# Optimization experiments

Measured on AMD Instinct MI355X. Metric: run time of the kernel, lower is better.

## Reference

```python
import jax, jax.numpy as jnp
import numpy as np

N, E = 50000, 800000
IN, EIN, HID, OUT = 128, 64, 64, 64
NEG_SLOPE = 0.2


def setup_inputs() -> dict:
    key = jax.random.key(0)
    ks = jax.random.split(key, 24)
    p = lambda k, shape: jax.random.normal(k, shape, jnp.float32) * 0.05
    return {
        'x': jax.random.normal(ks[0], (N, IN), jnp.float32),
        'edge_index': jax.random.randint(ks[1], (2, E), 0, N, jnp.int64),
        'edge_attr': jax.random.normal(ks[2], (E, EIN), jnp.float32),
        'batch': jnp.sort(jax.random.randint(ks[3], (N,), 0, 64, jnp.int64)),
        # GATConv 1 (in -> hidden, edge_dim=EIN)
        'W1': p(ks[4], (IN, HID)), 'a_src1': p(ks[5], (HID,)), 'a_dst1': p(ks[6], (HID,)),
        'We1': p(ks[7], (EIN, HID)), 'a_e1': p(ks[8], (HID,)), 'b1': jnp.zeros((HID,), jnp.float32),
        # GATConv 2 (hidden -> out)
        'W2': p(ks[9], (HID, OUT)), 'a_src2': p(ks[10], (OUT,)), 'a_dst2': p(ks[11], (OUT,)),
        'We2': p(ks[12], (EIN, OUT)), 'a_e2': p(ks[13], (OUT,)), 'b2': jnp.zeros((OUT,), jnp.float32),
        # edge MLP
        'Wm1': p(ks[14], (EIN, HID)), 'bm1': jnp.zeros((HID,), jnp.float32),
        'Wm2': p(ks[15], (HID, OUT)), 'bm2': jnp.zeros((OUT,), jnp.float32),
    }


def _gat(x, src, dst, edge_attr, W, a_s, a_d, We, a_e, b, n):
    # PyG GATConv (heads=1): add self-loops with edge_attr fill_value='mean'
    ones = jnp.ones((src.shape[0],), x.dtype)
    deg = jax.ops.segment_sum(ones, dst, num_segments=n)
    loop_attr = jax.ops.segment_sum(edge_attr, dst, num_segments=n) / jnp.maximum(deg, 1.0)[:, None]
    ar = jnp.arange(n)
    src2 = jnp.concatenate([src, ar])
    dst2 = jnp.concatenate([dst, ar])
    ea = jnp.concatenate([edge_attr, loop_attr], axis=0)  # [E+N, EIN]
    h = x @ W                                             # [N, C]
    a_src = h @ a_s                                       # [N]
    a_dst = h @ a_d                                       # [N]
    a_edge = (ea @ We) @ a_e                              # [E+N]
    alpha = jax.nn.leaky_relu(a_src[src2] + a_dst[dst2] + a_edge, NEG_SLOPE)
    # scatter-softmax over incoming edges of each dst node
    amax = jax.ops.segment_max(alpha, dst2, num_segments=n)
    ex = jnp.exp(alpha - amax[dst2])
    denom = jax.ops.segment_sum(ex, dst2, num_segments=n)
    coef = ex / denom[dst2]                               # [E+N]
    out = jax.ops.segment_sum(h[src2] * coef[:, None], dst2, num_segments=n)
    return out + b


def reference(x, edge_index, edge_attr, batch,
              W1, a_src1, a_dst1, We1, a_e1, b1,
              W2, a_src2, a_dst2, We2, a_e2, b2,
              Wm1, bm1, Wm2, bm2):
    n = x.shape[0]
    src, dst = edge_index[0], edge_index[1]
    h = _gat(x, src, dst, edge_attr, W1, a_src1, a_dst1, We1, a_e1, b1, n)
    h = jax.nn.elu(h)
    h = _gat(h, src, dst, edge_attr, W2, a_src2, a_dst2, We2, a_e2, b2, n)
    e = jax.nn.relu(edge_attr @ Wm1 + bm1) @ Wm2 + bm2
    return h, e, batch
```

## Files before the change

### kernel.cpp

```cpp
#include <hip/hip_runtime.h>

constexpr int NN = 50000;
constexpr int NE = 800000;
constexpr int C = 64;
constexpr int IN_DIM = 128;
constexpr float NEG = 0.2f;
constexpr int NB = (NN + 255) / 256;

typedef __attribute__((ext_vector_type(8))) short short8;
typedef __attribute__((ext_vector_type(4))) float f32x4;

__device__ __forceinline__ unsigned short f2bf(float f) {
    unsigned u = __float_as_uint(f);
    unsigned r = 0x7FFFu + ((u >> 16) & 1u);
    return (unsigned short)((u + r) >> 16);
}
__device__ __forceinline__ unsigned pack_bf2(float a, float b) {
    return (unsigned)f2bf(a) | ((unsigned)f2bf(b) << 16);
}
__device__ __forceinline__ float bf2f(unsigned u) {
    return __uint_as_float(u << 16);
}

__global__ void k_zero(int* __restrict__ p, int n) {
    int t = blockIdx.x * blockDim.x + threadIdx.x;
    if (t < n) p[t] = 0;
}

__global__ void k_vecs(const float* __restrict__ We1, const float* __restrict__ ae1v,
                       const float* __restrict__ We2, const float* __restrict__ ae2v,
                       const float* __restrict__ W1, const float* __restrict__ as1,
                       const float* __restrict__ ad1,
                       const float* __restrict__ W2, const float* __restrict__ as2,
                       const float* __restrict__ ad2,
                       float* __restrict__ out) {
    int t = blockIdx.x * blockDim.x + threadIdx.x;
    const float* M; const float* v; int row;
    if      (t < 64)  { M = We1; v = ae1v; row = t; }
    else if (t < 128) { M = We2; v = ae2v; row = t - 64; }
    else if (t < 256) { M = W1;  v = as1;  row = t - 128; }
    else if (t < 384) { M = W1;  v = ad1;  row = t - 256; }
    else if (t < 448) { M = W2;  v = as2;  row = t - 384; }
    else              { M = W2;  v = ad2;  row = t - 448; }
    float s = 0.f;
    #pragma unroll
    for (int c = 0; c < 64; ++c) s += M[row * 64 + c] * v[c];
    out[t] = s;
}

__global__ __launch_bounds__(256) void k_mlp_mfma(
        const float* __restrict__ ea, const int* __restrict__ dst,
        const float* __restrict__ Wm1, const float* __restrict__ bm1,
        const float* __restrict__ Wm2, const float* __restrict__ bm2,
        const float* __restrict__ wv,
        float* __restrict__ eout, float* __restrict__ ae1, float* __restrict__ ae2,
        int* __restrict__ hist) {
    constexpr int AP = 144;
    __shared__ char Atile[128 * AP];
    __shared__ char Bt1[64 * AP];
    __shared__ char Bt2[64 * AP];
    const int t = threadIdx.x;
    const long long E0 = (long long)blockIdx.x * 128;
    const int l = t & 63;

    if (t < 128) atomicAdd(&hist[dst[E0 + t]], 1);

    {
        const int j = t & 15;
        const int eb = t >> 4;
        float4 wk1 = *(const float4*)&wv[j * 4];
        float4 wk2 = *(const float4*)&wv[64 + j * 4];
        const f32x4* g = (const f32x4*)(ea + E0 * 64);
        float s1[8], s2[8];
        #pragma unroll
        for (int q = 0; q < 8; ++q) {
            f32x4 v = __builtin_nontemporal_load(&g[t + 256 * q]);
            int e = eb + 16 * q;
            s1[q] = v[0] * wk1.x + v[1] * wk1.y + v[2] * wk1.z + v[3] * wk1.w;
            s2[q] = v[0] * wk2.x + v[1] * wk2.y + v[2] * wk2.z + v[3] * wk2.w;
            uint2 wr;
            wr.x = pack_bf2(v[0], v[1]);
            wr.y = pack_bf2(v[2], v[3]);
            *(uint2*)(Atile + e * AP + j * 8) = wr;
        }
        #pragma unroll
        for (int off = 1; off < 16; off <<= 1) {
            #pragma unroll
            for (int q = 0; q < 8; ++q) {
                s1[q] += __shfl_xor(s1[q], off);
                s2[q] += __shfl_xor(s2[q], off);
            }
        }
        float o1 = 0.f, o2 = 0.f;
        #pragma unroll
        for (int q = 0; q < 8; ++q) {
            if (j == q)     o1 = s1[q];
            if (j == q + 8) o2 = s2[q];
        }
        if (j < 8) ae1[E0 + eb + 16 * j] = o1;
        else       ae2[E0 + eb + 16 * (j - 8)] = o2;
    }
    {
        const int c = t & 63, kq = t >> 6;
        #pragma unroll
        for (int i = 0; i < 16; i += 2) {
            int k = kq * 16 + i;
            *(unsigned*)(Bt1 + c * AP + k * 2) = pack_bf2(Wm1[k * 64 + c], Wm1[(k + 1) * 64 + c]);
            *(unsigned*)(Bt2 + c * AP + k * 2) = pack_bf2(Wm2[k * 64 + c], Wm2[(k + 1) * 64 + c]);
        }
    }
    __syncthreads();

    const int m0 = (t >> 6) * 32;
    const int lr = l & 15;
    const int lq = l >> 4;
    const int lk = lq * 8;

    f32x4 acc[4][2] = {};
    #pragma unroll
    for (int ks = 0; ks < 2; ++ks) {
        int ko = ks * 32 + lk;
        short8 a0 = *(const short8*)(Atile + (m0 + lr) * AP + ko * 2);
        short8 a1 = *(const short8*)(Atile + (m0 + 16 + lr) * AP + ko * 2);
        #pragma unroll
        for (int ct = 0; ct < 4; ++ct) {
            short8 b = *(const short8*)(Bt1 + (ct * 16 + lr) * AP + ko * 2);
            acc[ct][0] = __builtin_amdgcn_mfma_f32_16x16x32_bf16(b, a0, acc[ct][0], 0, 0, 0);
            acc[ct][1] = __builtin_amdgcn_mfma_f32_16x16x32_bf16(b, a1, acc[ct][1], 0, 0, 0);
        }
    }
    #pragma unroll
    for (int ct = 0; ct < 4; ++ct) {
        float4 bv = *(const float4*)&bm1[ct * 16 + lq * 4];
        #pragma unroll
        for (int et = 0; et < 2; ++et) {
            float v0 = fmaxf(acc[ct][et][0] + bv.x, 0.f);
            float v1 = fmaxf(acc[ct][et][1] + bv.y, 0.f);
            float v2 = fmaxf(acc[ct][et][2] + bv.z, 0.f);
            float v3 = fmaxf(acc[ct][et][3] + bv.w, 0.f);
            uint2 w;
            w.x = pack_bf2(v0, v1);
            w.y = pack_bf2(v2, v3);
            int e = m0 + et * 16 + lr;
            *(uint2*)(Atile + e * AP + (ct * 16 + lq * 4) * 2) = w;
        }
    }
    f32x4 acc2[4][2] = {};
    #pragma unroll
    for (int ks = 0; ks < 2; ++ks) {
        int ko = ks * 32 + lk;
        short8 a0 = *(const short8*)(Atile + (m0 + lr) * AP + ko * 2);
        short8 a1 = *(const short8*)(Atile + (m0 + 16 + lr) * AP + ko * 2);
        #pragma unroll
        for (int ct = 0; ct < 4; ++ct) {
            short8 b = *(const short8*)(Bt2 + (ct * 16 + lr) * AP + ko * 2);
            acc2[ct][0] = __builtin_amdgcn_mfma_f32_16x16x32_bf16(b, a0, acc2[ct][0], 0, 0, 0);
            acc2[ct][1] = __builtin_amdgcn_mfma_f32_16x16x32_bf16(b, a1, acc2[ct][1], 0, 0, 0);
        }
    }
    #pragma unroll
    for (int ct = 0; ct < 4; ++ct) {
        float4 bv = *(const float4*)&bm2[ct * 16 + lq * 4];
        #pragma unroll
        for (int et = 0; et < 2; ++et) {
            int e = m0 + et * 16 + lr;
            f32x4 o;
            o[0] = acc2[ct][et][0] + bv.x;
            o[1] = acc2[ct][et][1] + bv.y;
            o[2] = acc2[ct][et][2] + bv.z;
            o[3] = acc2[ct][et][3] + bv.w;
            __builtin_nontemporal_store(o, (f32x4*)&eout[(E0 + e) * 64 + ct * 16 + lq * 4]);
        }
    }
}

template <int K>
__global__ __launch_bounds__(256) void k_feat_mfma(
        const float* __restrict__ x, const float* __restrict__ W,
        const float* __restrict__ uv,
        unsigned short* __restrict__ h, float* __restrict__ asrc,
        float* __restrict__ adst, int M) {
    constexpr int AP = K * 2 + 16;
    constexpr int QW = K / 4;
    constexpr int NQ = K / 8;
    constexpr int EPQ = 256 / QW;
    __shared__ char Atile[128 * AP];
    __shared__ char Bt[64 * AP];
    const int t = threadIdx.x;
    const int M0 = blockIdx.x * 128;
    const int l = t & 63;

    {
        const int j = t % QW;
        const int eb = t / QW;
        float4 wk1 = *(const float4*)&uv[j * 4];
        float4 wk2 = *(const float4*)&uv[K + j * 4];
        const float4* g = (const float4*)(x + (long long)M0 * K);
        float s1[NQ], s2[NQ];
        #pragma unroll
        for (int q = 0; q < NQ; ++q) {
            int e = eb + EPQ * q;
            float4 v = make_float4(0.f, 0.f, 0.f, 0.f);
            if (M0 + e < M) v = g[t + 256 * q];
            s1[q] = v.x * wk1.x + v.y * wk1.y + v.z * wk1.z + v.w * wk1.w;
            s2[q] = v.x * wk2.x + v.y * wk2.y + v.z * wk2.z + v.w * wk2.w;
            uint2 wr;
            wr.x = pack_bf2(v.x, v.y);
            wr.y = pack_bf2(v.z, v.w);
            *(uint2*)(Atile + e * AP + j * 8) = wr;
        }
        #pragma unroll
        for (int off = 1; off < QW; off <<= 1) {
            #pragma unroll
            for (int q = 0; q < NQ; ++q) {
                s1[q] += __shfl_xor(s1[q], off);
                s2[q] += __shfl_xor(s2[q], off);
            }
        }
        float o1 = 0.f, o2 = 0.f;
        #pragma unroll
        for (int q = 0; q < NQ; ++q) {
            if (j == q)      o1 = s1[q];
            if (j == q + NQ) o2 = s2[q];
        }
        if (j < NQ) { int e = eb + EPQ * j;        if (M0 + e < M) asrc[M0 + e] = o1; }
        else        { int e = eb + EPQ * (j - NQ); if (M0 + e < M) adst[M0 + e] = o2; }
    }
    {
        const int c = t & 63, kq = t >> 6;
        #pragma unroll
        for (int i = 0; i < K / 4; i += 2) {
            int k = kq * (K / 4) + i;
            *(unsigned*)(Bt + c * AP + k * 2) = pack_bf2(W[k * 64 + c], W[(k + 1) * 64 + c]);
        }
    }
    __syncthreads();

    const int m0 = (t >> 6) * 32;
    const int lr = l & 15;
    const int lq = l >> 4;
    const int lk = lq * 8;

    f32x4 acc[4][2] = {};
    #pragma unroll
    for (int ks = 0; ks < K / 32; ++ks) {
        int ko = ks * 32 + lk;
        short8 a0 = *(const short8*)(Atile + (m0 + lr) * AP + ko * 2);
        short8 a1 = *(const short8*)(Atile + (m0 + 16 + lr) * AP + ko * 2);
        #pragma unroll
        for (int ct = 0; ct < 4; ++ct) {
            short8 b = *(const short8*)(Bt + (ct * 16 + lr) * AP + ko * 2);
            acc[ct][0] = __builtin_amdgcn_mfma_f32_16x16x32_bf16(b, a0, acc[ct][0], 0, 0, 0);
            acc[ct][1] = __builtin_amdgcn_mfma_f32_16x16x32_bf16(b, a1, acc[ct][1], 0, 0, 0);
        }
    }
    #pragma unroll
    for (int ct = 0; ct < 4; ++ct)
    #pragma unroll
    for (int et = 0; et < 2; ++et) {
        int row = m0 + et * 16 + lr;
        if (M0 + row < M) {
            uint2 w;
            w.x = pack_bf2(acc[ct][et][0], acc[ct][et][1]);
            w.y = pack_bf2(acc[ct][et][2], acc[ct][et][3]);
            *(uint2*)&h[(long long)(M0 + row) * 64 + ct * 16 + lq * 4] = w;
        }
    }
}

__global__ void k_scan1(const int* __restrict__ hist, int* __restrict__ row_ptr,
                        int* __restrict__ bsum) {
    __shared__ int s[256];
    int t = threadIdx.x;
    int idx = blockIdx.x * 256 + t;
    int v = (idx < NN) ? hist[idx] : 0;
    s[t] = v;
    __syncthreads();
    #pragma unroll
    for (int off = 1; off < 256; off <<= 1) {
        int x = (t >= off) ? s[t - off] : 0;
        __syncthreads();
        s[t] += x;
        __syncthreads();
    }
    if (idx < NN) row_ptr[idx] = s[t] - v;
    if (t == 255) bsum[blockIdx.x] = s[255];
}

__global__ void k_scan2(int* __restrict__ bsum) {
    __shared__ int s[256];
    int t = threadIdx.x;
    int v = (t < NB) ? bsum[t] : 0;
    s[t] = v;
    __syncthreads();
    #pragma unroll
    for (int off = 1; off < 256; off <<= 1) {
        int x = (t >= off) ? s[t - off] : 0;
        __syncthreads();
        s[t] += x;
        __syncthreads();
    }
    if (t < NB) bsum[t] = s[t] - v;
}

__global__ void k_scan3(const int* __restrict__ bsum, int* __restrict__ row_ptr,
                        int* __restrict__ cursor) {
    int idx = blockIdx.x * 256 + threadIdx.x;
    if (idx < NN) {
        int r = row_ptr[idx] + bsum[blockIdx.x];
        row_ptr[idx] = r;
        cursor[idx] = r;
    }
    if (idx == 0) row_ptr[NN] = NE;
}

__global__ void k_scatter(const int* __restrict__ src, const int* __restrict__ dst,
                          const float* __restrict__ ae1, const float* __restrict__ ae2,
                          int* __restrict__ cursor, uint2* __restrict__ csr) {
    int t = blockIdx.x * blockDim.x + threadIdx.x;
    if (t >= NE) return;
    int d = dst[t];
    int pos = atomicAdd(&cursor[d], 1);
    csr[pos] = make_uint2((unsigned)src[t], pack_bf2(ae1[t], ae2[t]));
}

template <bool IS_L1>
__global__ void k_gat(const int* __restrict__ row_ptr, const uint2* __restrict__ csr,
                      const float* __restrict__ asrc, const float* __restrict__ adst,
                      const unsigned short* __restrict__ h, const float* __restrict__ bias,
                      float* __restrict__ out) {
    int n = blockIdx.x * 4 + (threadIdx.x >> 6);
    if (n >= NN) return;
    int lane = threadIdx.x & 63;
    int g = lane >> 4, s = lane & 15;
    int beg = row_ptr[n], end = row_ptr[n + 1];
    float adn = adst[n];
    float m = -1e30f, l = 0.f, sum_ae = 0.f;
    float4 acc = make_float4(0.f, 0.f, 0.f, 0.f);

    int i = beg + g;
    uint2 rc = make_uint2(0u, 0u);
    ushort4 hu = make_ushort4(0, 0, 0, 0);
    float asv = 0.f;
    if (i < end) {
        rc = csr[i];
        hu = *(const ushort4*)&h[(long long)rc.x * 64 + s * 4];
        asv = asrc[rc.x];
    }
    for (; i < end; i += 4) {
        uint2 rn = rc; ushort4 hn = hu; float asn = asv;
        if (i + 4 < end) {
            rn = csr[i + 4];
            hn = *(const ushort4*)&h[(long long)rn.x * 64 + s * 4];
            asn = asrc[rn.x];
        }
        float ae = IS_L1 ? bf2f(rc.y & 0xFFFFu) : bf2f(rc.y >> 16);
        sum_ae += ae;
        float a = asv + adn + ae;
        a = a > 0.f ? a : NEG * a;
        float mn = fmaxf(m, a);
        float sc = __expf(m - mn), p = __expf(a - mn);
        l = l * sc + p;
        acc.x = acc.x * sc + p * bf2f(hu.x);
        acc.y = acc.y * sc + p * bf2f(hu.y);
        acc.z = acc.z * sc + p * bf2f(hu.z);
        acc.w = acc.w * sc + p * bf2f(hu.w);
        m = mn;
        rc = rn; hu = hn; asv = asn;
    }
    #pragma unroll
    for (int off = 16; off < 64; off <<= 1) {
        float mo = __shfl_xor(m, off);
        float lo = __shfl_xor(l, off);
        float ax = __shfl_xor(acc.x, off);
        float ay = __shfl_xor(acc.y, off);
        float az = __shfl_xor(acc.z, off);
        float aw = __shfl_xor(acc.w, off);
        float so = __shfl_xor(sum_ae, off);
        float mn = fmaxf(m, mo);
        float s1 = __expf(m - mn), s2 = __expf(mo - mn);
        l = l * s1 + lo * s2;
        acc.x = acc.x * s1 + ax * s2;
        acc.y = acc.y * s1 + ay * s2;
        acc.z = acc.z * s1 + az * s2;
        acc.w = acc.w * s1 + aw * s2;
        sum_ae += so;
        m = mn;
    }
    {
        float deg = (float)(end - beg);
        float ae = sum_ae / fmaxf(deg, 1.f);
        float a = asrc[n] + adn + ae;
        a = a > 0.f ? a : NEG * a;
        ushort4 hun = *(const ushort4*)&h[(long long)n * 64 + s * 4];
        float mn = fmaxf(m, a);
        float sc = __expf(m - mn), p = __expf(a - mn);
        l = l * sc + p;
        acc.x = acc.x * sc + p * bf2f(hun.x);
        acc.y = acc.y * sc + p * bf2f(hun.y);
        acc.z = acc.z * sc + p * bf2f(hun.z);
        acc.w = acc.w * sc + p * bf2f(hun.w);
    }
    if (g == 0) {
        float4 o;
        o.x = acc.x / l + bias[s * 4 + 0];
        o.y = acc.y / l + bias[s * 4 + 1];
        o.z = acc.z / l + bias[s * 4 + 2];
        o.w = acc.w / l + bias[s * 4 + 3];
        if (IS_L1) {
            o.x = o.x > 0.f ? o.x : expm1f(o.x);
            o.y = o.y > 0.f ? o.y : expm1f(o.y);
            o.z = o.z > 0.f ? o.z : expm1f(o.z);
            o.w = o.w > 0.f ? o.w : expm1f(o.w);
        }
        *(float4*)&out[(long long)n * 64 + s * 4] = o;
    }
}

__global__ void k_batch(const int* __restrict__ batch, float* __restrict__ out) {
    int t = blockIdx.x * blockDim.x + threadIdx.x;
    if (t >= NN) return;
    out[t] = (float)batch[t];
}

extern "C" void kernel_launch(void* const* d_in, const int* in_sizes, int n_in,
                              void* d_out, int out_size, void* d_ws, size_t ws_size,
                              hipStream_t stream) {
    const float* x     = (const float*)d_in[0];
    const int*   eidx  = (const int*)d_in[1];
    const float* eattr = (const float*)d_in[2];
    const int*   batch = (const int*)d_in[3];
    const float* W1 = (const float*)d_in[4];
    const float* as1 = (const float*)d_in[5];
    const float* ad1 = (const float*)d_in[6];
    const float* We1 = (const float*)d_in[7];
    const float* vae1 = (const float*)d_in[8];
    const float* b1  = (const float*)d_in[9];
    const float* W2 = (const float*)d_in[10];
    const float* as2 = (const float*)d_in[11];
    const float* ad2 = (const float*)d_in[12];
    const float* We2 = (const float*)d_in[13];
    const float* vae2 = (const float*)d_in[14];
    const float* b2  = (const float*)d_in[15];
    const float* Wm1 = (const float*)d_in[16];
    const float* bm1 = (const float*)d_in[17];
    const float* Wm2 = (const float*)d_in[18];
    const float* bm2 = (const float*)d_in[19];

    const int* src = eidx;
    const int* dst = eidx + NE;

    float* out_h = (float*)d_out;
    float* out_e = out_h + (long long)NN * C;
    float* out_b = out_e + (long long)NE * C;

    uint2* csr    = (uint2*)d_ws;
    float* ae1    = (float*)(csr + NE);
    float* ae2    = ae1 + NE;
    float* out1   = ae2 + NE;
    unsigned short* h = (unsigned short*)(out1 + (long long)NN * C);
    float* asrc   = (float*)(h + (long long)NN * C);
    float* adst   = asrc + NN;
    float* vecs   = adst + NN;
    int*   hist   = (int*)(vecs + 512);
    int*   row_ptr= hist + NN;
    int*   cursor = row_ptr + NN + 1;
    int*   bsum   = cursor + NN;

    k_zero<<<NB, 256, 0, stream>>>(hist, NN);

    k_vecs<<<2, 256, 0, stream>>>(We1, vae1, We2, vae2, W1, as1, ad1, W2, as2, ad2, vecs);

    k_mlp_mfma<<<NE / 128, 256, 0, stream>>>(eattr, dst, Wm1, bm1, Wm2, bm2, vecs,
                                             out_e, ae1, ae2, hist);

    k_scan1<<<NB, 256, 0, stream>>>(hist, row_ptr, bsum);
    k_scan2<<<1, 256, 0, stream>>>(bsum);
    k_scan3<<<NB, 256, 0, stream>>>(bsum, row_ptr, cursor);
    k_scatter<<<(NE + 255) / 256, 256, 0, stream>>>(src, dst, ae1, ae2, cursor, csr);

    k_feat_mfma<IN_DIM><<<(NN + 127) / 128, 256, 0, stream>>>(x, W1, vecs + 128,
                                                              h, asrc, adst, NN);
    k_gat<true><<<(NN + 3) / 4, 256, 0, stream>>>(row_ptr, csr, asrc, adst, h, b1, out1);

    k_feat_mfma<C><<<(NN + 127) / 128, 256, 0, stream>>>(out1, W2, vecs + 384,
                                                         h, asrc, adst, NN);
    k_gat<false><<<(NN + 3) / 4, 256, 0, stream>>>(row_ptr, csr, asrc, adst, h, b2, out_h);

    k_batch<<<(NN + 255) / 256, 256, 0, stream>>>(batch, out_b);
}
```

Before: 279.8 us.

## Fuse setup kernels, single-pass scan with lookback, bf16 layer-1 output

Merges histogram zeroing, attention vector precompute and batch output into one setup kernel. Replaces the three-kernel prefix scan with a single kernel where each block publishes its aggregate and waits on its predecessors' flags. Stores the first GAT layer output in bf16 so the second feature GEMM reads half the bytes. This cuts kernel launches and intermediate traffic, at the cost of relying on all scan blocks being co-resident and a small precision loss in the hidden activations.

```diff
diff --git a/kernel.cpp b/kernel.cpp
--- a/kernel.cpp
+++ b/kernel.cpp
@@ -22,30 +22,32 @@
     return __uint_as_float(u << 16);
 }
 
-__global__ void k_zero(int* __restrict__ p, int n) {
-    int t = blockIdx.x * blockDim.x + threadIdx.x;
-    if (t < n) p[t] = 0;
-}
-
-__global__ void k_vecs(const float* __restrict__ We1, const float* __restrict__ ae1v,
-                       const float* __restrict__ We2, const float* __restrict__ ae2v,
-                       const float* __restrict__ W1, const float* __restrict__ as1,
-                       const float* __restrict__ ad1,
-                       const float* __restrict__ W2, const float* __restrict__ as2,
-                       const float* __restrict__ ad2,
-                       float* __restrict__ out) {
-    int t = blockIdx.x * blockDim.x + threadIdx.x;
-    const float* M; const float* v; int row;
-    if      (t < 64)  { M = We1; v = ae1v; row = t; }
-    else if (t < 128) { M = We2; v = ae2v; row = t - 64; }
-    else if (t < 256) { M = W1;  v = as1;  row = t - 128; }
-    else if (t < 384) { M = W1;  v = ad1;  row = t - 256; }
-    else if (t < 448) { M = W2;  v = as2;  row = t - 384; }
-    else              { M = W2;  v = ad2;  row = t - 448; }
-    float s = 0.f;
-    #pragma unroll
-    for (int c = 0; c < 64; ++c) s += M[row * 64 + c] * v[c];
-    out[t] = s;
+__global__ __launch_bounds__(256) void k_setup(
+        const float* __restrict__ We1, const float* __restrict__ ae1v,
+        const float* __restrict__ We2, const float* __restrict__ ae2v,
+        const float* __restrict__ W1, const float* __restrict__ as1,
+        const float* __restrict__ ad1,
+        const float* __restrict__ W2, const float* __restrict__ as2,
+        const float* __restrict__ ad2,
+        const int* __restrict__ batch,
+        float* __restrict__ vecs, int* __restrict__ hist, int* __restrict__ bagg,
+        float* __restrict__ out_b) {
+    int t = blockIdx.x * 256 + threadIdx.x;
+    if (t < 512) {
+        const float* M; const float* v; int row;
+        if      (t < 64)  { M = We1; v = ae1v; row = t; }
+        else if (t < 128) { M = We2; v = ae2v; row = t - 64; }
+        else if (t < 256) { M = W1;  v = as1;  row = t - 128; }
+        else if (t < 384) { M = W1;  v = ad1;  row = t - 256; }
+        else if (t < 448) { M = W2;  v = as2;  row = t - 384; }
+        else              { M = W2;  v = ad2;  row = t - 448; }
+        float s = 0.f;
+        #pragma unroll
+        for (int c = 0; c < 64; ++c) s += M[row * 64 + c] * v[c];
+        vecs[t] = s;
+    }
+    if (t < NN) { hist[t] = 0; out_b[t] = (float)batch[t]; }
+    if (t < NB) bagg[t] = 0;
 }
 
 __global__ __launch_bounds__(256) void k_mlp_mfma(
@@ -174,9 +176,9 @@
     }
 }
 
-template <int K>
+template <int K, bool BF16IN>
 __global__ __launch_bounds__(256) void k_feat_mfma(
-        const float* __restrict__ x, const float* __restrict__ W,
+        const void* __restrict__ xv, const float* __restrict__ W,
         const float* __restrict__ uv,
         unsigned short* __restrict__ h, float* __restrict__ asrc,
         float* __restrict__ adst, int M) {
@@ -195,18 +197,29 @@
         const int eb = t / QW;
         float4 wk1 = *(const float4*)&uv[j * 4];
         float4 wk2 = *(const float4*)&uv[K + j * 4];
-        const float4* g = (const float4*)(x + (long long)M0 * K);
         float s1[NQ], s2[NQ];
         #pragma unroll
         for (int q = 0; q < NQ; ++q) {
             int e = eb + EPQ * q;
-            float4 v = make_float4(0.f, 0.f, 0.f, 0.f);
-            if (M0 + e < M) v = g[t + 256 * q];
-            s1[q] = v.x * wk1.x + v.y * wk1.y + v.z * wk1.z + v.w * wk1.w;
-            s2[q] = v.x * wk2.x + v.y * wk2.y + v.z * wk2.z + v.w * wk2.w;
+            float v0, v1, v2, v3;
             uint2 wr;
-            wr.x = pack_bf2(v.x, v.y);
-            wr.y = pack_bf2(v.z, v.w);
+            if constexpr (BF16IN) {
+                const uint2* g = (const uint2*)xv + (long long)M0 * (K / 4);
+                uint2 w = make_uint2(0u, 0u);
+                if (M0 + e < M) w = g[t + 256 * q];
+                v0 = bf2f(w.x & 0xFFFFu); v1 = bf2f(w.x >> 16);
+                v2 = bf2f(w.y & 0xFFFFu); v3 = bf2f(w.y >> 16);
+                wr = w;
+            } else {
+                const float4* g = (const float4*)xv + (long long)M0 * (K / 4);
+                float4 v = make_float4(0.f, 0.f, 0.f, 0.f);
+                if (M0 + e < M) v = g[t + 256 * q];
+                v0 = v.x; v1 = v.y; v2 = v.z; v3 = v.w;
+                wr.x = pack_bf2(v.x, v.y);
+                wr.y = pack_bf2(v.z, v.w);
+            }
+            s1[q] = v0 * wk1.x + v1 * wk1.y + v2 * wk1.z + v3 * wk1.w;
+            s2[q] = v0 * wk2.x + v1 * wk2.y + v2 * wk2.z + v3 * wk2.w;
             *(uint2*)(Atile + e * AP + j * 8) = wr;
         }
         #pragma unroll
@@ -268,11 +281,12 @@
     }
 }
 
-__global__ void k_scan1(const int* __restrict__ hist, int* __restrict__ row_ptr,
-                        int* __restrict__ bsum) {
+__global__ __launch_bounds__(256) void k_scan_f(const int* __restrict__ hist,
+        int* __restrict__ row_ptr, int* __restrict__ cursor, int* __restrict__ bagg) {
     __shared__ int s[256];
-    int t = threadIdx.x;
-    int idx = blockIdx.x * 256 + t;
+    __shared__ int red[5];
+    const int t = threadIdx.x, b = blockIdx.x;
+    const int idx = b * 256 + t;
     int v = (idx < NN) ? hist[idx] : 0;
     s[t] = v;
     __syncthreads();
@@ -283,35 +297,30 @@
         s[t] += x;
         __syncthreads();
     }
-    if (idx < NN) row_ptr[idx] = s[t] - v;
-    if (t == 255) bsum[blockIdx.x] = s[255];
-}
-
-__global__ void k_scan2(int* __restrict__ bsum) {
-    __shared__ int s[256];
-    int t = threadIdx.x;
-    int v = (t < NB) ? bsum[t] : 0;
-    s[t] = v;
+    if (t == 255)
+        __hip_atomic_store(&bagg[b], (s[255] << 1) | 1,
+                           __ATOMIC_RELEASE, __HIP_MEMORY_SCOPE_AGENT);
+    int contrib = 0;
+    if (t < b) {
+        int a;
+        do {
+            a = __hip_atomic_load(&bagg[t], __ATOMIC_ACQUIRE, __HIP_MEMORY_SCOPE_AGENT);
+        } while (!(a & 1));
+        contrib = a >> 1;
+    }
+    #pragma unroll
+    for (int off = 32; off; off >>= 1) contrib += __shfl_down(contrib, off);
+    if ((t & 63) == 0) red[t >> 6] = contrib;
     __syncthreads();
-    #pragma unroll
-    for (int off = 1; off < 256; off <<= 1) {
-        int x = (t >= off) ? s[t - off] : 0;
-        __syncthreads();
-        s[t] += x;
-        __syncthreads();
-    }
-    if (t < NB) bsum[t] = s[t] - v;
-}
-
-__global__ void k_scan3(const int* __restrict__ bsum, int* __restrict__ row_ptr,
-                        int* __restrict__ cursor) {
-    int idx = blockIdx.x * 256 + threadIdx.x;
+    if (t == 0) red[4] = red[0] + red[1] + red[2] + red[3];
+    __syncthreads();
+    int offset = red[4];
     if (idx < NN) {
-        int r = row_ptr[idx] + bsum[blockIdx.x];
-        row_ptr[idx] = r;
-        cursor[idx] = r;
-    }
-    if (idx == 0) row_ptr[NN] = NE;
+        int rp = offset + s[t] - v;
+        row_ptr[idx] = rp;
+        cursor[idx] = rp;
+    }
+    if (idx == NN) row_ptr[NN] = NE;
 }
 
 __global__ void k_scatter(const int* __restrict__ src, const int* __restrict__ dst,
@@ -328,7 +337,7 @@
 __global__ void k_gat(const int* __restrict__ row_ptr, const uint2* __restrict__ csr,
                       const float* __restrict__ asrc, const float* __restrict__ adst,
                       const unsigned short* __restrict__ h, const float* __restrict__ bias,
-                      float* __restrict__ out) {
+                      void* __restrict__ outv) {
     int n = blockIdx.x * 4 + (threadIdx.x >> 6);
     if (n >= NN) return;
     int lane = threadIdx.x & 63;
@@ -412,15 +421,14 @@
             o.y = o.y > 0.f ? o.y : expm1f(o.y);
             o.z = o.z > 0.f ? o.z : expm1f(o.z);
             o.w = o.w > 0.f ? o.w : expm1f(o.w);
-        }
-        *(float4*)&out[(long long)n * 64 + s * 4] = o;
-    }
-}
-
-__global__ void k_batch(const int* __restrict__ batch, float* __restrict__ out) {
-    int t = blockIdx.x * blockDim.x + threadIdx.x;
-    if (t >= NN) return;
-    out[t] = (float)batch[t];
+            uint2 w;
+            w.x = pack_bf2(o.x, o.y);
+            w.y = pack_bf2(o.z, o.w);
+            *(uint2*)&((unsigned short*)outv)[(long long)n * 64 + s * 4] = w;
+        } else {
+            *(float4*)&((float*)outv)[(long long)n * 64 + s * 4] = o;
+        }
+    }
 }
 
 extern "C" void kernel_launch(void* const* d_in, const int* in_sizes, int n_in,
@@ -457,35 +465,30 @@
     uint2* csr    = (uint2*)d_ws;
     float* ae1    = (float*)(csr + NE);
     float* ae2    = ae1 + NE;
-    float* out1   = ae2 + NE;
-    unsigned short* h = (unsigned short*)(out1 + (long long)NN * C);
+    unsigned short* out1b = (unsigned short*)(ae2 + NE);
+    unsigned short* h = out1b + (long long)NN * C;
     float* asrc   = (float*)(h + (long long)NN * C);
     float* adst   = asrc + NN;
     float* vecs   = adst + NN;
     int*   hist   = (int*)(vecs + 512);
     int*   row_ptr= hist + NN;
     int*   cursor = row_ptr + NN + 1;
-    int*   bsum   = cursor + NN;
-
-    k_zero<<<NB, 256, 0, stream>>>(hist, NN);
-
-    k_vecs<<<2, 256, 0, stream>>>(We1, vae1, We2, vae2, W1, as1, ad1, W2, as2, ad2, vecs);
+    int*   bagg   = cursor + NN;
+
+    k_setup<<<NB, 256, 0, stream>>>(We1, vae1, We2, vae2, W1, as1, ad1,
+                                    W2, as2, ad2, batch, vecs, hist, bagg, out_b);
 
     k_mlp_mfma<<<NE / 128, 256, 0, stream>>>(eattr, dst, Wm1, bm1, Wm2, bm2, vecs,
                                              out_e, ae1, ae2, hist);
 
-    k_scan1<<<NB, 256, 0, stream>>>(hist, row_ptr, bsum);
-    k_scan2<<<1, 256, 0, stream>>>(bsum);
-    k_scan3<<<NB, 256, 0, stream>>>(bsum, row_ptr, cursor);
+    k_scan_f<<<NB, 256, 0, stream>>>(hist, row_ptr, cursor, bagg);
     k_scatter<<<(NE + 255) / 256, 256, 0, stream>>>(src, dst, ae1, ae2, cursor, csr);
 
-    k_feat_mfma<IN_DIM><<<(NN + 127) / 128, 256, 0, stream>>>(x, W1, vecs + 128,
-                                                              h, asrc, adst, NN);
-    k_gat<true><<<(NN + 3) / 4, 256, 0, stream>>>(row_ptr, csr, asrc, adst, h, b1, out1);
-
-    k_feat_mfma<C><<<(NN + 127) / 128, 256, 0, stream>>>(out1, W2, vecs + 384,
-                                                         h, asrc, adst, NN);
+    k_feat_mfma<IN_DIM, false><<<(NN + 127) / 128, 256, 0, stream>>>(x, W1, vecs + 128,
+                                                                     h, asrc, adst, NN);
+    k_gat<true><<<(NN + 3) / 4, 256, 0, stream>>>(row_ptr, csr, asrc, adst, h, b1, out1b);
+
+    k_feat_mfma<C, true><<<(NN + 127) / 128, 256, 0, stream>>>(out1b, W2, vecs + 384,
+                                                               h, asrc, adst, NN);
     k_gat<false><<<(NN + 3) / 4, 256, 0, stream>>>(row_ptr, csr, asrc, adst, h, b2, out_h);
-
-    k_batch<<<(NN + 255) / 256, 256, 0, stream>>>(batch, out_b);
-}
+}
```

Measured after the change: 281.2 us. Within noise of the previous version (+0.5%).
